# Kernel optimization log

Measured on AMD Instinct MI355X. Metric: run time of the kernel, lower is better.

Reference implementation:

```python
import jax, jax.numpy as jnp
import numpy as np

N_NODES = 100000
F_IN = 128


def gcn_conv(x, W, b, src, dst, num_nodes):
    """PyG GCNConv: add self-loops, symmetric deg^-1/2 normalization,
    aggregate then linear (equivalently linear then aggregate)."""
    h = x @ W  # [N, F_out]
    # self-loops
    loop = jnp.arange(num_nodes, dtype=src.dtype)
    s = jnp.concatenate([src, loop])
    d = jnp.concatenate([dst, loop])
    ones = jnp.ones(s.shape[0], dtype=x.dtype)
    deg = jax.ops.segment_sum(ones, d, num_segments=num_nodes)  # in-degree w/ self-loops
    dinv = jnp.where(deg > 0, jax.lax.rsqrt(deg), 0.0)
    norm = dinv[s] * dinv[d]  # [E+N]
    msg = h[s] * norm[:, None]  # gather + scale
    out = jax.ops.segment_sum(msg, d, num_segments=num_nodes)  # scatter-add
    return out + b


def setup_inputs() -> dict:
    key = jax.random.key(0)
    k1, k2, k3, k4 = jax.random.split(key, 4)
    x = jax.random.normal(k1, (N_NODES, F_IN), dtype=jnp.float32)
    edge_index = jax.random.randint(k2, (2, 600000), 0, N_NODES, dtype=jnp.int64)
    # GCNConv weights (glorot-ish scale) and zero biases
    W1 = jax.random.normal(k3, (F_IN, F_IN), dtype=jnp.float32) / np.sqrt(F_IN)
    b1 = jnp.zeros((F_IN,), dtype=jnp.float32)
    W2 = jax.random.normal(k4, (F_IN, 2 * F_IN), dtype=jnp.float32) / np.sqrt(F_IN)
    b2 = jnp.zeros((2 * F_IN,), dtype=jnp.float32)
    return {"x": x, "edge_index": edge_index, "W1": W1, "b1": b1, "W2": W2, "b2": b2}


def reference(x, edge_index, W1, b1, W2, b2):
    src, dst = edge_index[0], edge_index[1]
    n = x.shape[0]
    h = gcn_conv(x, W1, b1, src, dst, n)
    h = jax.nn.relu(h)  # dropout is identity in eval mode
    h = gcn_conv(h, W2, b2, src, dst, n)
    h = jax.nn.relu(h)
    return jnp.mean(h, axis=0)  # [2*F_IN]
```

## Files before the change

### kernel.cpp

```cpp
#include <hip/hip_runtime.h>


typedef __attribute__((ext_vector_type(8))) short short8;
typedef __attribute__((ext_vector_type(4))) float f32x4;

__device__ __forceinline__ float b2f(unsigned short u) {
    union { unsigned int i; float f; } c;
    c.i = ((unsigned int)u) << 16;
    return c.f;
}
__device__ __forceinline__ unsigned short f2b(float x) {
    union { float f; unsigned int i; } c;
    c.f = x;
    unsigned int r = c.i + 0x7FFFu + ((c.i >> 16) & 1u);
    return (unsigned short)(r >> 16);
}

__global__ void k_detect(const int* __restrict__ ei, int E, int* __restrict__ flag) {
    __shared__ int anyv[4];
    int t = threadIdx.x;
    int v = 0;
#pragma unroll
    for (int r = 0; r < 4; ++r) {
        long long k = (long long)(t * 4 + r) * E >> 10;
        v |= ei[2 * (int)k + 1];
    }
    unsigned long long m = __ballot(v != 0);
    if ((t & 63) == 0) anyv[t >> 6] = (m != 0ull) ? 1 : 0;
    __syncthreads();
    if (t == 0) flag[0] = anyv[0] | anyv[1] | anyv[2] | anyv[3];
}

__device__ __forceinline__ int edge_idx(const void* ei, int is64, int which,
                                        int E, int e) {
    if (is64) return (int)((const long long*)ei)[(size_t)which * E + e];
    return ((const int*)ei)[(size_t)which * E + e];
}

__global__ void k_count(const void* __restrict__ ei, const int* __restrict__ flag,
                        int* __restrict__ counts, int E) {
    int e = blockIdx.x * 256 + threadIdx.x;
    if (e >= E) return;
    int is64 = (*flag == 0);
    int d = edge_idx(ei, is64, 1, E, e);
    atomicAdd(&counts[d], 1);
}

__global__ void k_scan1(const int* __restrict__ counts, int* __restrict__ offs,
                        int* __restrict__ blockSums, float* __restrict__ dinv,
                        int n) {
    __shared__ int tmp[256];
    int t = threadIdx.x;
    int i = blockIdx.x * 256 + t;
    int my = (i < n) ? counts[i] : 0;
    if (i < n) dinv[i] = rsqrtf(1.0f + (float)my);
    tmp[t] = my;
    __syncthreads();
    for (int off = 1; off < 256; off <<= 1) {
        int v = (t >= off) ? tmp[t - off] : 0;
        __syncthreads();
        tmp[t] += v;
        __syncthreads();
    }
    if (i < n) offs[i] = tmp[t] - my;
    if (t == 255) blockSums[blockIdx.x] = tmp[255];
}

__global__ void k_scan2(int* __restrict__ blockSums, int nb) {
    __shared__ int tmp[512];
    __shared__ int carry;
    int t = threadIdx.x;
    if (t == 0) carry = 0;
    __syncthreads();
    for (int base = 0; base < nb; base += 512) {
        int i = base + t;
        int my = (i < nb) ? blockSums[i] : 0;
        tmp[t] = my;
        __syncthreads();
        for (int off = 1; off < 512; off <<= 1) {
            int v = (t >= off) ? tmp[t - off] : 0;
            __syncthreads();
            tmp[t] += v;
            __syncthreads();
        }
        if (i < nb) blockSums[i] = carry + tmp[t] - my;
        __syncthreads();
        if (t == 0) carry += tmp[511];
        __syncthreads();
    }
}

__global__ void k_scan3(int* __restrict__ offs, const int* __restrict__ blockSums,
                        int* __restrict__ cursor, int n) {
    int i = blockIdx.x * 256 + threadIdx.x;
    if (i < n) {
        int o = offs[i] + blockSums[blockIdx.x];
        offs[i] = o;
        cursor[i] = o;
    }
}

__global__ void k_fill_csr(const void* __restrict__ ei, const int* __restrict__ flag,
                           const float* __restrict__ dinv, int* __restrict__ cursor,
                           int2* __restrict__ csr2, int E) {
    int e = blockIdx.x * 256 + threadIdx.x;
    if (e >= E) return;
    int is64 = (*flag == 0);
    int s = edge_idx(ei, is64, 0, E, e);
    int d = edge_idx(ei, is64, 1, E, e);
    int pos = atomicAdd(&cursor[d], 1);
    csr2[pos] = make_int2(s, __float_as_int(dinv[s] * dinv[d]));
}

__global__ void k_cvt_x(const float* __restrict__ x, unsigned short* __restrict__ xb,
                        int n4) {
    int i = blockIdx.x * 256 + threadIdx.x;
    if (i >= n4) return;
    float4 v = reinterpret_cast<const float4*>(x)[i];
    ushort4 o;
    o.x = f2b(v.x); o.y = f2b(v.y); o.z = f2b(v.z); o.w = f2b(v.w);
    reinterpret_cast<ushort4*>(xb)[i] = o;
}

__global__ void k_cvt_wt(const float* __restrict__ W, unsigned short* __restrict__ WT,
                         int KOUT, int total) {
    int idx = blockIdx.x * 256 + threadIdx.x;
    if (idx >= total) return;
    int k = idx / KOUT, n = idx % KOUT;
    WT[(size_t)n * 128 + k] = f2b(W[idx]);
}

template <int CHUNK>
__global__ __launch_bounds__(256) void k_gather_b(const unsigned short* __restrict__ h,
                                                  const float* __restrict__ dinv,
                                                  const int* __restrict__ offs,
                                                  const int* __restrict__ counts,
                                                  const int2* __restrict__ csr2,
                                                  unsigned short* __restrict__ g,
                                                  int N) {
    const int grp = threadIdx.x >> 4, l16 = threadIdx.x & 15;
    const short8* h8 = reinterpret_cast<const short8*>(h);
    const int base = blockIdx.x * (CHUNK * 16) + grp;

    for (int i = 0; i < CHUNK; ++i) {
        const int node = base + i * 16;
        if (node >= N) break;
        const float dd = dinv[node];
        const float w0 = dd * dd;
        const size_t rowu = (size_t)node * 16 + l16;
        short8 sv = h8[rowu];
        float a[8];
#pragma unroll
        for (int j = 0; j < 8; ++j) a[j] = b2f((unsigned short)sv[j]) * w0;

        const int beg = offs[node], cnt = counts[node];
        if (cnt > 0) {
            int2 p = csr2[beg];
            short8 v = h8[(size_t)p.x * 16 + l16];
            for (int e = 1; e < cnt; ++e) {
                int2 pn = csr2[beg + e];
                short8 vn = h8[(size_t)pn.x * 16 + l16];
                float w = __int_as_float(p.y);
#pragma unroll
                for (int j = 0; j < 8; ++j)
                    a[j] = fmaf(b2f((unsigned short)v[j]), w, a[j]);
                p = pn; v = vn;
            }
            float w = __int_as_float(p.y);
#pragma unroll
            for (int j = 0; j < 8; ++j)
                a[j] = fmaf(b2f((unsigned short)v[j]), w, a[j]);
        }
        short8 o;
#pragma unroll
        for (int j = 0; j < 8; ++j) o[j] = (short)f2b(a[j]);
        reinterpret_cast<short8*>(g)[rowu] = o;
    }
}

template <int KOUT, bool REDUCE, int CHUNK>
__global__ __launch_bounds__(256) void k_mgemm(const unsigned short* __restrict__ A,
                                               const unsigned short* __restrict__ WT,
                                               const float* __restrict__ bias,
                                               unsigned short* __restrict__ C,
                                               float* __restrict__ partials, int N) {
    constexpr int NFW = KOUT / 64;
    const int tid = threadIdx.x;
    const int wave = tid >> 6, lane = tid & 63;
    const int l15 = lane & 15, lg = lane >> 4;
    const int colbase = wave * (KOUT / 4);

    short8 breg[NFW][4];
    float bv[NFW];
#pragma unroll
    for (int nf = 0; nf < NFW; ++nf) {
        int col = colbase + nf * 16 + l15;
        bv[nf] = bias[col];
#pragma unroll
        for (int kk = 0; kk < 4; ++kk)
            breg[nf][kk] = *reinterpret_cast<const short8*>(
                WT + (size_t)col * 128 + kk * 32 + lg * 8);
    }

    float psum[NFW];
#pragma unroll
    for (int nf = 0; nf < NFW; ++nf) psum[nf] = 0.f;

    const int NT = (N + 15) / 16;
    const int t0 = blockIdx.x * CHUNK;
    const int tend = (t0 + CHUNK < NT) ? t0 + CHUNK : NT;

#pragma unroll 2
    for (int t = t0; t < tend; ++t) {
        const int rows = t * 16;
        const int arow = rows + l15;
        short8 a[4];
        const bool rv = arow < N;
#pragma unroll
        for (int kk = 0; kk < 4; ++kk)
            a[kk] = rv ? *reinterpret_cast<const short8*>(
                             A + (size_t)arow * 128 + kk * 32 + lg * 8)
                       : (short8){0, 0, 0, 0, 0, 0, 0, 0};

        f32x4 acc[NFW];
#pragma unroll
        for (int nf = 0; nf < NFW; ++nf) acc[nf] = (f32x4){0.f, 0.f, 0.f, 0.f};
#pragma unroll
        for (int kk = 0; kk < 4; ++kk)
#pragma unroll
            for (int nf = 0; nf < NFW; ++nf)
                acc[nf] = __builtin_amdgcn_mfma_f32_16x16x32_bf16(
                    a[kk], breg[nf][kk], acc[nf], 0, 0, 0);

        if (!REDUCE) {
#pragma unroll
            for (int nf = 0; nf < NFW; ++nf) {
                int col = colbase + nf * 16 + l15;
#pragma unroll
                for (int r = 0; r < 4; ++r) {
                    int rr = rows + lg * 4 + r;
                    if (rr < N)
                        C[(size_t)rr * KOUT + col] =
                            f2b(fmaxf(acc[nf][r] + bv[nf], 0.f));
                }
            }
        } else {
#pragma unroll
            for (int nf = 0; nf < NFW; ++nf) {
#pragma unroll
                for (int r = 0; r < 4; ++r) {
                    int rr = rows + lg * 4 + r;
                    if (rr < N) psum[nf] += fmaxf(acc[nf][r] + bv[nf], 0.f);
                }
            }
        }
    }

    if (REDUCE) {
#pragma unroll
        for (int nf = 0; nf < NFW; ++nf) {
            float s = psum[nf];
            s += __shfl_xor(s, 16);
            s += __shfl_xor(s, 32);
            if (lg == 0)
                partials[(size_t)blockIdx.x * KOUT + colbase + nf * 16 + l15] = s;
        }
    }
}

__global__ void k_reduce1(const float* __restrict__ partials, float* __restrict__ p2,
                          int NB) {
    int c = threadIdx.x;
    float sum = 0.f;
    for (int r = blockIdx.x; r < NB; r += 16)
        sum += partials[(size_t)r * 256 + c];
    p2[blockIdx.x * 256 + c] = sum;
}

__global__ void k_reduce2(const float* __restrict__ p2, float* __restrict__ out,
                          float invN) {
    int c = threadIdx.x;
    float sum = 0.f;
#pragma unroll
    for (int b = 0; b < 16; ++b) sum += p2[b * 256 + c];
    out[c] = sum * invN;
}

extern "C" void kernel_launch(void* const* d_in, const int* in_sizes, int n_in,
                              void* d_out, int out_size, void* d_ws, size_t ws_size,
                              hipStream_t stream) {
    const float* x  = (const float*)d_in[0];
    const void*  ei = d_in[1];
    const float* W1 = (const float*)d_in[2];
    const float* b1 = (const float*)d_in[3];
    const float* W2 = (const float*)d_in[4];
    const float* b2 = (const float*)d_in[5];
    float* out = (float*)d_out;

    const int N = in_sizes[0] / 128;
    const int E = in_sizes[1] / 2;
    const int nb = (N + 255) / 256;
    constexpr int GCHUNK = 4;
    constexpr int MCHUNK = 8;
    const int NT = (N + 15) / 16;
    const int NBLK = (NT + MCHUNK - 1) / MCHUNK;
    const int GBLK = (N + GCHUNK * 16 - 1) / (GCHUNK * 16);

    char* ws = (char*)d_ws;
    size_t off = 0;
    auto alloc = [&](size_t bytes) {
        char* p = ws + off;
        off += (bytes + 255) & ~(size_t)255;
        return p;
    };
    int*            flag      = (int*)alloc(4);
    int*            counts    = (int*)alloc((size_t)N * 4);
    int*            offs      = (int*)alloc((size_t)N * 4);
    int*            cursor    = (int*)alloc((size_t)N * 4);
    int*            blockSums = (int*)alloc((size_t)nb * 4);
    float*          dinv      = (float*)alloc((size_t)N * 4);
    int2*           csr2      = (int2*)alloc((size_t)E * 8);
    float*          partials  = (float*)alloc((size_t)NBLK * 256 * 4);
    float*          p2        = (float*)alloc((size_t)16 * 256 * 4);
    unsigned short* wt1       = (unsigned short*)alloc((size_t)128 * 128 * 2);
    unsigned short* wt2       = (unsigned short*)alloc((size_t)256 * 128 * 2);
    unsigned short* xb        = (unsigned short*)alloc((size_t)N * 128 * 2);
    unsigned short* g1        = (unsigned short*)alloc((size_t)N * 128 * 2);
    unsigned short* a1r       = (unsigned short*)alloc((size_t)N * 128 * 2);
    unsigned short* g2        = xb;

    k_detect<<<1, 256, 0, stream>>>((const int*)ei, E, flag);
    hipMemsetAsync(counts, 0, (size_t)N * 4, stream);
    k_count<<<(E + 255) / 256, 256, 0, stream>>>(ei, flag, counts, E);
    k_scan1<<<nb, 256, 0, stream>>>(counts, offs, blockSums, dinv, N);
    k_scan2<<<1, 512, 0, stream>>>(blockSums, nb);
    k_scan3<<<nb, 256, 0, stream>>>(offs, blockSums, cursor, N);
    k_fill_csr<<<(E + 255) / 256, 256, 0, stream>>>(ei, flag, dinv, cursor, csr2, E);

    k_cvt_x<<<(N * 32 + 255) / 256, 256, 0, stream>>>(x, xb, N * 32);
    k_cvt_wt<<<(128 * 128 + 255) / 256, 256, 0, stream>>>(W1, wt1, 128, 128 * 128);
    k_cvt_wt<<<(128 * 256 + 255) / 256, 256, 0, stream>>>(W2, wt2, 256, 128 * 256);

    k_gather_b<GCHUNK><<<GBLK, 256, 0, stream>>>(xb, dinv, offs, counts, csr2, g1, N);
    k_mgemm<128, false, MCHUNK><<<NBLK, 256, 0, stream>>>(g1, wt1, b1, a1r, nullptr, N);

    k_gather_b<GCHUNK><<<GBLK, 256, 0, stream>>>(a1r, dinv, offs, counts, csr2, g2, N);
    k_mgemm<256, true, MCHUNK><<<NBLK, 256, 0, stream>>>(g2, wt2, b2, nullptr, partials, N);
    k_reduce1<<<16, 256, 0, stream>>>(partials, p2, NBLK);
    k_reduce2<<<1, 256, 0, stream>>>(p2, out, 1.0f / (float)N);
}
```

Measured before the change: 219.5 us.

## Split each node's edge gather across four slots per wave; merge setup launches

The gather kernel now assigns one wavefront per node. The node's incoming edges are split across four 16-lane slots, and partial sums are combined with cross-lane shuffles, instead of one 16-lane group walking every edge serially. The aim is more memory-level parallelism on the random row loads, since average degree is about six. The detect and memset steps are folded into one init kernel, and the two weight conversions are merged into one launch to cut launch overhead. The cost is fewer nodes per block, shuffle reductions, and idle slots on low-degree nodes.

```diff
diff --git a/kernel.cpp b/kernel.cpp
--- a/kernel.cpp
+++ b/kernel.cpp
@@ -16,25 +16,30 @@
     return (unsigned short)(r >> 16);
 }
 
-__global__ void k_detect(const int* __restrict__ ei, int E, int* __restrict__ flag) {
-    __shared__ int anyv[4];
-    int t = threadIdx.x;
-    int v = 0;
-#pragma unroll
-    for (int r = 0; r < 4; ++r) {
-        long long k = (long long)(t * 4 + r) * E >> 10;
-        v |= ei[2 * (int)k + 1];
-    }
-    unsigned long long m = __ballot(v != 0);
-    if ((t & 63) == 0) anyv[t >> 6] = (m != 0ull) ? 1 : 0;
-    __syncthreads();
-    if (t == 0) flag[0] = anyv[0] | anyv[1] | anyv[2] | anyv[3];
-}
-
 __device__ __forceinline__ int edge_idx(const void* ei, int is64, int which,
                                         int E, int e) {
     if (is64) return (int)((const long long*)ei)[(size_t)which * E + e];
     return ((const int*)ei)[(size_t)which * E + e];
+}
+
+__global__ void k_init(const int* __restrict__ ei, int E, int* __restrict__ counts,
+                       int* __restrict__ flag, int N) {
+    int i = blockIdx.x * 256 + threadIdx.x;
+    if (i < N) counts[i] = 0;
+    if (blockIdx.x == 0) {
+        __shared__ int anyv[4];
+        int t = threadIdx.x;
+        int v = 0;
+#pragma unroll
+        for (int r = 0; r < 4; ++r) {
+            long long k = (long long)(t * 4 + r) * E >> 10;
+            v |= ei[2 * (int)k + 1];
+        }
+        unsigned long long m = __ballot(v != 0);
+        if ((t & 63) == 0) anyv[t >> 6] = (m != 0ull) ? 1 : 0;
+        __syncthreads();
+        if (t == 0) flag[0] = anyv[0] | anyv[1] | anyv[2] | anyv[3];
+    }
 }
 
 __global__ void k_count(const void* __restrict__ ei, const int* __restrict__ flag,
@@ -122,12 +127,18 @@
     reinterpret_cast<ushort4*>(xb)[i] = o;
 }
 
-__global__ void k_cvt_wt(const float* __restrict__ W, unsigned short* __restrict__ WT,
-                         int KOUT, int total) {
+__global__ void k_cvt_w(const float* __restrict__ W1, const float* __restrict__ W2,
+                        unsigned short* __restrict__ wt1,
+                        unsigned short* __restrict__ wt2) {
     int idx = blockIdx.x * 256 + threadIdx.x;
-    if (idx >= total) return;
-    int k = idx / KOUT, n = idx % KOUT;
-    WT[(size_t)n * 128 + k] = f2b(W[idx]);
+    if (idx < 128 * 128) {
+        int k = idx >> 7, n = idx & 127;
+        wt1[(size_t)n * 128 + k] = f2b(W1[idx]);
+    } else if (idx < 128 * 128 + 128 * 256) {
+        int i2 = idx - 128 * 128;
+        int k = i2 >> 8, n = i2 & 255;
+        wt2[(size_t)n * 128 + k] = f2b(W2[i2]);
+    }
 }
 
 template <int CHUNK>
@@ -138,43 +149,44 @@
                                                   const int2* __restrict__ csr2,
                                                   unsigned short* __restrict__ g,
                                                   int N) {
-    const int grp = threadIdx.x >> 4, l16 = threadIdx.x & 15;
+    const int wid = threadIdx.x >> 6;
+    const int slot = (threadIdx.x >> 4) & 3;
+    const int l16 = threadIdx.x & 15;
     const short8* h8 = reinterpret_cast<const short8*>(h);
-    const int base = blockIdx.x * (CHUNK * 16) + grp;
+    const int start = blockIdx.x * (CHUNK * 4);
 
     for (int i = 0; i < CHUNK; ++i) {
-        const int node = base + i * 16;
-        if (node >= N) break;
-        const float dd = dinv[node];
-        const float w0 = dd * dd;
+        const int node = start + i * 4 + wid;
+        if (node >= N) continue;
+        float a[8] = {0.f, 0.f, 0.f, 0.f, 0.f, 0.f, 0.f, 0.f};
         const size_t rowu = (size_t)node * 16 + l16;
-        short8 sv = h8[rowu];
-        float a[8];
-#pragma unroll
-        for (int j = 0; j < 8; ++j) a[j] = b2f((unsigned short)sv[j]) * w0;
-
+        if (slot == 0) {
+            const float dd = dinv[node];
+            const float w0 = dd * dd;
+            short8 sv = h8[rowu];
+#pragma unroll
+            for (int j = 0; j < 8; ++j) a[j] = b2f((unsigned short)sv[j]) * w0;
+        }
         const int beg = offs[node], cnt = counts[node];
-        if (cnt > 0) {
-            int2 p = csr2[beg];
+        for (int e = slot; e < cnt; e += 4) {
+            int2 p = csr2[beg + e];
             short8 v = h8[(size_t)p.x * 16 + l16];
-            for (int e = 1; e < cnt; ++e) {
-                int2 pn = csr2[beg + e];
-                short8 vn = h8[(size_t)pn.x * 16 + l16];
-                float w = __int_as_float(p.y);
-#pragma unroll
-                for (int j = 0; j < 8; ++j)
-                    a[j] = fmaf(b2f((unsigned short)v[j]), w, a[j]);
-                p = pn; v = vn;
-            }
             float w = __int_as_float(p.y);
 #pragma unroll
             for (int j = 0; j < 8; ++j)
                 a[j] = fmaf(b2f((unsigned short)v[j]), w, a[j]);
         }
-        short8 o;
-#pragma unroll
-        for (int j = 0; j < 8; ++j) o[j] = (short)f2b(a[j]);
-        reinterpret_cast<short8*>(g)[rowu] = o;
+#pragma unroll
+        for (int j = 0; j < 8; ++j) {
+            a[j] += __shfl_xor(a[j], 16);
+            a[j] += __shfl_xor(a[j], 32);
+        }
+        if (slot == 0) {
+            short8 o;
+#pragma unroll
+            for (int j = 0; j < 8; ++j) o[j] = (short)f2b(a[j]);
+            reinterpret_cast<short8*>(g)[rowu] = o;
+        }
     }
 }
 
@@ -304,7 +316,7 @@
     constexpr int MCHUNK = 8;
     const int NT = (N + 15) / 16;
     const int NBLK = (NT + MCHUNK - 1) / MCHUNK;
-    const int GBLK = (N + GCHUNK * 16 - 1) / (GCHUNK * 16);
+    const int GBLK = (N + GCHUNK * 4 - 1) / (GCHUNK * 4);
 
     char* ws = (char*)d_ws;
     size_t off = 0;
@@ -329,8 +341,7 @@
     unsigned short* a1r       = (unsigned short*)alloc((size_t)N * 128 * 2);
     unsigned short* g2        = xb;
 
-    k_detect<<<1, 256, 0, stream>>>((const int*)ei, E, flag);
-    hipMemsetAsync(counts, 0, (size_t)N * 4, stream);
+    k_init<<<nb, 256, 0, stream>>>((const int*)ei, E, counts, flag, N);
     k_count<<<(E + 255) / 256, 256, 0, stream>>>(ei, flag, counts, E);
     k_scan1<<<nb, 256, 0, stream>>>(counts, offs, blockSums, dinv, N);
     k_scan2<<<1, 512, 0, stream>>>(blockSums, nb);
@@ -338,8 +349,7 @@
     k_fill_csr<<<(E + 255) / 256, 256, 0, stream>>>(ei, flag, dinv, cursor, csr2, E);
 
     k_cvt_x<<<(N * 32 + 255) / 256, 256, 0, stream>>>(x, xb, N * 32);
-    k_cvt_wt<<<(128 * 128 + 255) / 256, 256, 0, stream>>>(W1, wt1, 128, 128 * 128);
-    k_cvt_wt<<<(128 * 256 + 255) / 256, 256, 0, stream>>>(W2, wt2, 256, 128 * 256);
+    k_cvt_w<<<(128 * 384 + 255) / 256, 256, 0, stream>>>(W1, W2, wt1, wt2);
 
     k_gather_b<GCHUNK><<<GBLK, 256, 0, stream>>>(xb, dinv, offs, counts, csr2, g1, N);
     k_mgemm<128, false, MCHUNK><<<NBLK, 256, 0, stream>>>(g1, wt1, b1, a1r, nullptr, N);
```

New measurement: 240.1 us. 1.09x slower.
